# Kernel tuning notes

Measured on AMD Instinct MI355X. Metric: run time of the kernel, lower is better.

Reference implementation:

```python
import jax, jax.numpy as jnp
import numpy as np

EPS = 1e-5  # torch nn.LayerNorm default

def layer_norm(x, g, b):
    mu = jnp.mean(x, axis=-1, keepdims=True)
    var = jnp.mean((x - mu) ** 2, axis=-1, keepdims=True)  # biased, as torch
    return (x - mu) * jax.lax.rsqrt(var + EPS) * g + b

def quantum_circuit(v):
    # RX(v_w) per wire -> <Z_w> = cos(v_w); RZ(params) is diagonal phase (no effect
    # on Z probabilities); CNOT chain makes bit w = XOR of bits 0..w, hence
    # <Z_w> = prod_{k<=w} cos(v_k). Exact closed form of the PennyLane circuit.
    return jnp.cumprod(jnp.cos(v), axis=-1)

def setup_inputs() -> dict:
    key = jax.random.key(0)
    ks = jax.random.split(key, 8)
    B, T, C, H = 4, 2048, 1024, 16
    dk = C // H           # n_qubits_transformer
    nq_ffn, ffn_dim = 16, 4096
    return {
        "x": jax.random.normal(ks[0], (B, T, C), dtype=jnp.float32) * 0.5,
        "attn_circuit_params": jax.random.normal(ks[1], (H, dk), dtype=jnp.float32),
        "ffn_circuit_params": jax.random.normal(ks[2], (nq_ffn,), dtype=jnp.float32),
        "w1": jax.random.normal(ks[3], (ffn_dim, nq_ffn), dtype=jnp.float32) * 0.1,
        "b1": jnp.zeros((ffn_dim,), dtype=jnp.float32),
        "w2": jax.random.normal(ks[4], (C, ffn_dim), dtype=jnp.float32) * 0.02,
        "b2": jnp.zeros((C,), dtype=jnp.float32),
        "gamma1": jnp.ones((C,), dtype=jnp.float32),
        "beta1": jnp.zeros((C,), dtype=jnp.float32),
        "gamma2": jnp.ones((C,), dtype=jnp.float32),
        "beta2": jnp.zeros((C,), dtype=jnp.float32),
    }

def reference(x, attn_circuit_params, ffn_circuit_params, w1, b1, w2, b2,
              gamma1, beta1, gamma2, beta2):
    B, T, C = x.shape
    H, dk = attn_circuit_params.shape  # dk == n_qubits_transformer == C // H
    nq = ffn_circuit_params.shape[0]
    # --- quantum attention: per-head circuit over d_k wires (RZ params drop out) ---
    xh = x.reshape(B, T, H, dk)
    attn_out = quantum_circuit(xh).reshape(B, T, C)
    x1 = layer_norm(x + attn_out, gamma1, beta1)  # dropout = identity (eval)
    # --- quantum FFN: circuit on first nq channels of each token ---
    q = quantum_circuit(x1[..., :nq])                      # [B,T,nq]
    h = jnp.einsum('btq,fq->btf', q, w1) + b1              # [B,T,ffn_dim]
    ffn_out = jnp.einsum('btf,cf->btc', jax.nn.relu(h), w2) + b2
    return layer_norm(x1 + ffn_out, gamma2, beta2)
```

## Files before the change

### kernel.cpp

```cpp
#include <hip/hip_runtime.h>

#define M_TOK 8192
#define C_DIM 1024
#define F_DIM 4096
#define NQ    16

typedef __attribute__((ext_vector_type(8))) short short8v;
typedef __attribute__((ext_vector_type(4))) float f32x4;

typedef __attribute__((address_space(1))) void as1_void;
typedef __attribute__((address_space(3))) void as3_void;

__device__ __forceinline__ void gld_lds16(const void* g, void* l) {
  __builtin_amdgcn_global_load_lds((as1_void*)g, (as3_void*)l, 16, 0, 0);
}

__device__ __forceinline__ unsigned short f2bf(float f) {
  unsigned int u = __float_as_uint(f);
  u += 0x7FFFu + ((u >> 16) & 1u);
  return (unsigned short)(u >> 16);
}

__device__ __forceinline__ void mfma_16x16x32_bf16(f32x4& d, short8v a, short8v b) {
  asm("v_mfma_f32_16x16x32_bf16 %0, %1, %2, %0" : "+v"(d) : "v"(a), "v"(b));
}

__global__ __launch_bounds__(256) void k_attn_ln1(
    const float* __restrict__ x, const float* __restrict__ g1,
    const float* __restrict__ be1, float* __restrict__ x1,
    float* __restrict__ qf) {
  const int row  = blockIdx.x;
  const int tid  = threadIdx.x;
  const int lane = tid & 63;
  const int w    = tid >> 6;
  const float* xr = x + (size_t)row * C_DIM;

  float y[4];
  float s1 = 0.f, s2 = 0.f;
#pragma unroll
  for (int hi = 0; hi < 4; ++hi) {
    const int idx = (w * 4 + hi) * 64 + lane;
    const float v = xr[idx];
    float p = cosf(v);
#pragma unroll
    for (int off = 1; off < 64; off <<= 1) {
      const float up = __shfl_up(p, off, 64);
      if (lane >= off) p *= up;
    }
    const float yy = v + p;
    y[hi] = yy;
    s1 += yy;
    s2 += yy * yy;
  }
#pragma unroll
  for (int off = 32; off; off >>= 1) {
    s1 += __shfl_xor(s1, off, 64);
    s2 += __shfl_xor(s2, off, 64);
  }
  __shared__ float red[8];
  if (lane == 0) { red[w] = s1; red[4 + w] = s2; }
  __syncthreads();
  s1 = red[0] + red[1] + red[2] + red[3];
  s2 = red[4] + red[5] + red[6] + red[7];
  const float mu  = s1 * (1.f / C_DIM);
  const float var = s2 * (1.f / C_DIM) - mu * mu;
  const float rs  = rsqrtf(var + 1e-5f);

  float* x1r = x1 + (size_t)row * C_DIM;
#pragma unroll
  for (int hi = 0; hi < 4; ++hi) {
    const int idx = (w * 4 + hi) * 64 + lane;
    const float xv = (y[hi] - mu) * rs * g1[idx] + be1[idx];
    x1r[idx] = xv;
    if (w == 0 && hi == 0) {
      const float c = cosf(xv);
      float run = 1.f, mine = 0.f;
#pragma unroll
      for (int k = 0; k < NQ; ++k) {
        const float ck = __shfl(c, k, 64);
        run *= ck;
        if (lane == k) mine = run;
      }
      if (lane < NQ) qf[(size_t)row * NQ + lane] = mine;
    }
  }
}

__global__ __launch_bounds__(256) void k_w2cast(const float* __restrict__ w2,
                                                unsigned short* __restrict__ w2b) {
  const int n4 = C_DIM * F_DIM / 4;
  for (int i = blockIdx.x * 256 + threadIdx.x; i < n4; i += gridDim.x * 256) {
    const float4 v = ((const float4*)w2)[i];
    unsigned long long pk = (unsigned long long)f2bf(v.x)
                          | ((unsigned long long)f2bf(v.y) << 16)
                          | ((unsigned long long)f2bf(v.z) << 32)
                          | ((unsigned long long)f2bf(v.w) << 48);
    ((unsigned long long*)w2b)[i] = pk;
  }
}

__global__ __launch_bounds__(256) void k_ffn1(
    const float* __restrict__ qf, const float* __restrict__ w1,
    const float* __restrict__ b1, unsigned short* __restrict__ R) {
  const int tid  = threadIdx.x;
  const int lane = tid & 63;
  const int wv   = tid >> 6;
  const int r16  = lane & 15;
  const int hk   = lane >> 4;
  const int mb   = blockIdx.x * 16;
  const int fb   = blockIdx.y * 64 + wv * 16;

  short8v a = short8v{0,0,0,0,0,0,0,0};
  short8v b = short8v{0,0,0,0,0,0,0,0};
  if (hk < 2) {
    const float* qa = qf + (size_t)(mb + r16) * NQ + hk * 8;
    const float4 a0 = *(const float4*)(qa);
    const float4 a1 = *(const float4*)(qa + 4);
    a[0] = (short)f2bf(a0.x); a[1] = (short)f2bf(a0.y);
    a[2] = (short)f2bf(a0.z); a[3] = (short)f2bf(a0.w);
    a[4] = (short)f2bf(a1.x); a[5] = (short)f2bf(a1.y);
    a[6] = (short)f2bf(a1.z); a[7] = (short)f2bf(a1.w);
    const float* wb = w1 + (size_t)(fb + r16) * NQ + hk * 8;
    const float4 b0 = *(const float4*)(wb);
    const float4 b1v = *(const float4*)(wb + 4);
    b[0] = (short)f2bf(b0.x); b[1] = (short)f2bf(b0.y);
    b[2] = (short)f2bf(b0.z); b[3] = (short)f2bf(b0.w);
    b[4] = (short)f2bf(b1v.x); b[5] = (short)f2bf(b1v.y);
    b[6] = (short)f2bf(b1v.z); b[7] = (short)f2bf(b1v.w);
  }

  f32x4 acc = {0.f, 0.f, 0.f, 0.f};
  mfma_16x16x32_bf16(acc, a, b);

  const int f = fb + r16;
  const float bn = b1[f];
#pragma unroll
  for (int r = 0; r < 4; ++r) {
    const int m = mb + hk * 4 + r;
    R[(size_t)m * F_DIM + f] = f2bf(fmaxf(acc[r] + bn, 0.f));
  }
}

#define BM 256
#define BN 128
#define BK 64
#define NT (F_DIM / BK)
#define ATILE (BM * BK)
#define BTILE (BN * BK)
#define TILE3 (ATILE + BTILE)

__global__ __launch_bounds__(512) void k_gemm(
    const unsigned short* __restrict__ R, const unsigned short* __restrict__ W2,
    const float* __restrict__ b2, float* __restrict__ xio, int m_off) {
  __shared__ unsigned short L[3 * TILE3];
  const int tid = threadIdx.x;
  const int m0 = blockIdx.x * BM;
  const int n0 = blockIdx.y * BN;
  const unsigned short* Ag = R + (size_t)m0 * F_DIM;
  const unsigned short* Bg = W2 + (size_t)n0 * F_DIM;

  const int lane = tid & 63;
  const int wv  = tid >> 6;
  const int wr  = wv >> 1;
  const int wc  = wv & 1;
  const int r16 = lane & 15;
  const int hk  = lane >> 4;
  const int ar0 = wr * 64 + r16;
  const int br0 = wc * 64 + r16;

  f32x4 acc[4][4];
  const f32x4 fzero = {0.f, 0.f, 0.f, 0.f};
#pragma unroll
  for (int i = 0; i < 4; ++i)
#pragma unroll
    for (int j = 0; j < 4; ++j) acc[i][j] = fzero;

  auto stageA = [&](int c, int t, int l) {
    const int idx = l * 512 + tid;
    const int row = idx >> 3, slot = idx & 7;
    gld_lds16(Ag + (size_t)row * F_DIM + t * BK + ((slot ^ (row & 7)) << 3),
              &L[c * TILE3 + idx * 8]);
  };
  auto stageB = [&](int c, int t, int l) {
    const int idx = l * 512 + tid;
    const int row = idx >> 3, slot = idx & 7;
    gld_lds16(Bg + (size_t)row * F_DIM + t * BK + ((slot ^ (row & 7)) << 3),
              &L[c * TILE3 + ATILE + idx * 8]);
  };
  auto rdA = [&](int c, int row, int ks) {
    return *(const short8v*)&L[c * TILE3 + row * BK + ((ks ^ (row & 7)) << 3)];
  };
  auto rdB = [&](int c, int row, int ks) {
    return *(const short8v*)&L[c * TILE3 + ATILE + row * BK + ((ks ^ (row & 7)) << 3)];
  };

#pragma unroll
  for (int l = 0; l < 4; ++l) stageA(0, 0, l);
#pragma unroll
  for (int l = 0; l < 2; ++l) stageB(0, 0, l);
#pragma unroll
  for (int l = 0; l < 4; ++l) stageA(1, 1, l);
#pragma unroll
  for (int l = 0; l < 2; ++l) stageB(1, 1, l);
  asm volatile("s_waitcnt vmcnt(6)" ::: "memory");
  __builtin_amdgcn_s_barrier();

  for (int t = 0; t < NT; ++t) {
    const int cur = t % 3;
    const int nx2 = (t + 2) % 3;
    const bool pf = (t + 2) < NT;
    short8v a[4], b[4];

#pragma unroll
    for (int i = 0; i < 4; ++i) a[i] = rdA(cur, ar0 + i * 16, hk);
#pragma unroll
    for (int j = 0; j < 4; ++j) b[j] = rdB(cur, br0 + j * 16, hk);
    if (pf) { stageA(nx2, t + 2, 0); stageA(nx2, t + 2, 1); stageB(nx2, t + 2, 0); }
    __builtin_amdgcn_s_barrier();
    __builtin_amdgcn_s_setprio(1);
#pragma unroll
    for (int i = 0; i < 4; ++i)
#pragma unroll
      for (int j = 0; j < 4; ++j)
        mfma_16x16x32_bf16(acc[i][j], a[i], b[j]);
    __builtin_amdgcn_s_setprio(0);
    __builtin_amdgcn_s_barrier();

#pragma unroll
    for (int i = 0; i < 4; ++i) a[i] = rdA(cur, ar0 + i * 16, hk + 4);
#pragma unroll
    for (int j = 0; j < 4; ++j) b[j] = rdB(cur, br0 + j * 16, hk + 4);
    if (pf) { stageA(nx2, t + 2, 2); stageA(nx2, t + 2, 3); stageB(nx2, t + 2, 1); }
    __builtin_amdgcn_s_barrier();
    __builtin_amdgcn_s_setprio(1);
#pragma unroll
    for (int i = 0; i < 4; ++i)
#pragma unroll
      for (int j = 0; j < 4; ++j)
        mfma_16x16x32_bf16(acc[i][j], a[i], b[j]);
    __builtin_amdgcn_s_setprio(0);
    if (pf) asm volatile("s_waitcnt vmcnt(6)" ::: "memory");
    else    asm volatile("s_waitcnt vmcnt(0)" ::: "memory");
    __builtin_amdgcn_s_barrier();
  }

#pragma unroll
  for (int i = 0; i < 4; ++i) {
    const int gm = m_off + m0 + wr * 64 + i * 16 + hk * 4;
#pragma unroll
    for (int j = 0; j < 4; ++j) {
      const int n = n0 + wc * 64 + j * 16 + r16;
      const float bn = b2[n];
#pragma unroll
      for (int r = 0; r < 4; ++r) {
        const size_t off = (size_t)(gm + r) * C_DIM + n;
        xio[off] = acc[i][j][r] + bn + xio[off];
      }
    }
  }
}

__global__ __launch_bounds__(256) void k_ln2(float* __restrict__ y,
                                             const float* __restrict__ g2,
                                             const float* __restrict__ be2) {
  const int row = blockIdx.x;
  const int tid = threadIdx.x;
  float* yr = y + (size_t)row * C_DIM;
  const float4 v = ((const float4*)yr)[tid];
  float s1 = v.x + v.y + v.z + v.w;
  float s2 = v.x * v.x + v.y * v.y + v.z * v.z + v.w * v.w;
#pragma unroll
  for (int off = 32; off; off >>= 1) {
    s1 += __shfl_xor(s1, off, 64);
    s2 += __shfl_xor(s2, off, 64);
  }
  __shared__ float red[8];
  const int lane = tid & 63, w = tid >> 6;
  if (lane == 0) { red[w] = s1; red[4 + w] = s2; }
  __syncthreads();
  s1 = red[0] + red[1] + red[2] + red[3];
  s2 = red[4] + red[5] + red[6] + red[7];
  const float mu  = s1 * (1.f / C_DIM);
  const float var = s2 * (1.f / C_DIM) - mu * mu;
  const float rs  = rsqrtf(var + 1e-5f);
  const float4 g = ((const float4*)g2)[tid];
  const float4 b = ((const float4*)be2)[tid];
  float4 o;
  o.x = (v.x - mu) * rs * g.x + b.x;
  o.y = (v.y - mu) * rs * g.y + b.y;
  o.z = (v.z - mu) * rs * g.z + b.z;
  o.w = (v.w - mu) * rs * g.w + b.w;
  ((float4*)yr)[tid] = o;
}

extern "C" void kernel_launch(void* const* d_in, const int* in_sizes, int n_in,
                              void* d_out, int out_size, void* d_ws, size_t ws_size,
                              hipStream_t stream) {
  const float* x   = (const float*)d_in[0];
  const float* w1  = (const float*)d_in[3];
  const float* b1  = (const float*)d_in[4];
  const float* w2  = (const float*)d_in[5];
  const float* b2  = (const float*)d_in[6];
  const float* g1  = (const float*)d_in[7];
  const float* be1 = (const float*)d_in[8];
  const float* g2  = (const float*)d_in[9];
  const float* be2 = (const float*)d_in[10];
  float* out = (float*)d_out;

  char* ws = (char*)d_ws;
  float* qf = (float*)ws;
  unsigned short* w2b = (unsigned short*)(ws + 512 * 1024);
  const size_t rbase = 512 * 1024 + (size_t)8 * 1024 * 1024;
  unsigned short* Rb = (unsigned short*)(ws + rbase);

  int cm = M_TOK;
  const size_t avail = (ws_size > rbase) ? ws_size - rbase : 0;
  const size_t need = (size_t)M_TOK * F_DIM * 2;
  if (avail < need) {
    size_t rows = (avail / ((size_t)F_DIM * 2)) & ~(size_t)255;
    cm = (rows < 256) ? 256 : (int)rows;
  }

  k_attn_ln1<<<M_TOK, 256, 0, stream>>>(x, g1, be1, out, qf);
  k_w2cast<<<2048, 256, 0, stream>>>(w2, w2b);
  for (int c0 = 0; c0 < M_TOK; c0 += cm) {
    const int cur = (M_TOK - c0 < cm) ? (M_TOK - c0) : cm;
    k_ffn1<<<dim3(cur / 16, F_DIM / 64), 256, 0, stream>>>(
        qf + (size_t)c0 * NQ, w1, b1, Rb);
    k_gemm<<<dim3(cur / BM, C_DIM / BN), 512, 0, stream>>>(Rb, w2b, b2, out, c0);
  }
  k_ln2<<<M_TOK, 256, 0, stream>>>(out, g2, be2);
}
```

Measured before the change: 145.3 us.

## Split K across wave groups in the FFN GEMM and reduce through LDS

The waves of the second FFN GEMM are reorganised into two K-groups. Each group covers half of every BK slice and computes a 128x64 output sub-tile, instead of every wave computing a 64x64 sub-tile over the full BK. This cuts the LDS fragment reads per MFMA, issues all prefetch loads in one place, and removes a barrier from each K iteration. In exchange, the epilogue gains a cross-wave reduction through LDS and a __syncthreads. The accumulator doubles to 32 f32x4 per wave, which raises register pressure.

```diff
diff --git a/kernel.cpp b/kernel.cpp
--- a/kernel.cpp
+++ b/kernel.cpp
@@ -161,17 +161,20 @@
 
   const int lane = tid & 63;
   const int wv  = tid >> 6;
-  const int wr  = wv >> 1;
-  const int wc  = wv & 1;
+  const int kz  = wv >> 2;
+  const int wq  = wv & 3;
+  const int wr  = wq >> 1;
+  const int wc  = wq & 1;
   const int r16 = lane & 15;
   const int hk  = lane >> 4;
-  const int ar0 = wr * 64 + r16;
+  const int ks  = hk + kz * 4;
+  const int ar0 = wr * 128 + r16;
   const int br0 = wc * 64 + r16;
 
-  f32x4 acc[4][4];
+  f32x4 acc[8][4];
   const f32x4 fzero = {0.f, 0.f, 0.f, 0.f};
 #pragma unroll
-  for (int i = 0; i < 4; ++i)
+  for (int i = 0; i < 8; ++i)
 #pragma unroll
     for (int j = 0; j < 4; ++j) acc[i][j] = fzero;
 
@@ -187,11 +190,11 @@
     gld_lds16(Bg + (size_t)row * F_DIM + t * BK + ((slot ^ (row & 7)) << 3),
               &L[c * TILE3 + ATILE + idx * 8]);
   };
-  auto rdA = [&](int c, int row, int ks) {
-    return *(const short8v*)&L[c * TILE3 + row * BK + ((ks ^ (row & 7)) << 3)];
+  auto rdA = [&](int c, int row, int kg) {
+    return *(const short8v*)&L[c * TILE3 + row * BK + ((kg ^ (row & 7)) << 3)];
   };
-  auto rdB = [&](int c, int row, int ks) {
-    return *(const short8v*)&L[c * TILE3 + ATILE + row * BK + ((ks ^ (row & 7)) << 3)];
+  auto rdB = [&](int c, int row, int kg) {
+    return *(const short8v*)&L[c * TILE3 + ATILE + row * BK + ((kg ^ (row & 7)) << 3)];
   };
 
 #pragma unroll
@@ -209,32 +212,20 @@
     const int cur = t % 3;
     const int nx2 = (t + 2) % 3;
     const bool pf = (t + 2) < NT;
-    short8v a[4], b[4];
-
-#pragma unroll
-    for (int i = 0; i < 4; ++i) a[i] = rdA(cur, ar0 + i * 16, hk);
-#pragma unroll
-    for (int j = 0; j < 4; ++j) b[j] = rdB(cur, br0 + j * 16, hk);
-    if (pf) { stageA(nx2, t + 2, 0); stageA(nx2, t + 2, 1); stageB(nx2, t + 2, 0); }
-    __builtin_amdgcn_s_barrier();
+    short8v a[8], b[4];
+
+#pragma unroll
+    for (int i = 0; i < 8; ++i) a[i] = rdA(cur, ar0 + i * 16, ks);
+#pragma unroll
+    for (int j = 0; j < 4; ++j) b[j] = rdB(cur, br0 + j * 16, ks);
+    if (pf) {
+      stageA(nx2, t + 2, 0); stageA(nx2, t + 2, 1);
+      stageA(nx2, t + 2, 2); stageA(nx2, t + 2, 3);
+      stageB(nx2, t + 2, 0); stageB(nx2, t + 2, 1);
+    }
     __builtin_amdgcn_s_setprio(1);
 #pragma unroll
-    for (int i = 0; i < 4; ++i)
-#pragma unroll
-      for (int j = 0; j < 4; ++j)
-        mfma_16x16x32_bf16(acc[i][j], a[i], b[j]);
-    __builtin_amdgcn_s_setprio(0);
-    __builtin_amdgcn_s_barrier();
-
-#pragma unroll
-    for (int i = 0; i < 4; ++i) a[i] = rdA(cur, ar0 + i * 16, hk + 4);
-#pragma unroll
-    for (int j = 0; j < 4; ++j) b[j] = rdB(cur, br0 + j * 16, hk + 4);
-    if (pf) { stageA(nx2, t + 2, 2); stageA(nx2, t + 2, 3); stageB(nx2, t + 2, 1); }
-    __builtin_amdgcn_s_barrier();
-    __builtin_amdgcn_s_setprio(1);
-#pragma unroll
-    for (int i = 0; i < 4; ++i)
+    for (int i = 0; i < 8; ++i)
 #pragma unroll
       for (int j = 0; j < 4; ++j)
         mfma_16x16x32_bf16(acc[i][j], a[i], b[j]);
@@ -244,17 +235,32 @@
     __builtin_amdgcn_s_barrier();
   }
 
-#pragma unroll
-  for (int i = 0; i < 4; ++i) {
-    const int gm = m_off + m0 + wr * 64 + i * 16 + hk * 4;
-#pragma unroll
-    for (int j = 0; j < 4; ++j) {
-      const int n = n0 + wc * 64 + j * 16 + r16;
-      const float bn = b2[n];
-#pragma unroll
-      for (int r = 0; r < 4; ++r) {
-        const size_t off = (size_t)(gm + r) * C_DIM + n;
-        xio[off] = acc[i][j][r] + bn + xio[off];
+  float* Lf = (float*)L;
+  if (kz == 1) {
+#pragma unroll
+    for (int i = 0; i < 8; ++i)
+#pragma unroll
+      for (int j = 0; j < 4; ++j)
+#pragma unroll
+        for (int r = 0; r < 4; ++r)
+          Lf[wq * 8192 + (i * 16 + hk * 4 + r) * 64 + j * 16 + r16] = acc[i][j][r];
+  }
+  __syncthreads();
+
+  if (kz == 0) {
+#pragma unroll
+    for (int i = 0; i < 8; ++i) {
+      const int gm = m_off + m0 + wr * 128 + i * 16 + hk * 4;
+#pragma unroll
+      for (int j = 0; j < 4; ++j) {
+        const int n = n0 + wc * 64 + j * 16 + r16;
+        const float bn = b2[n];
+#pragma unroll
+        for (int r = 0; r < 4; ++r) {
+          const float part = Lf[wq * 8192 + (i * 16 + hk * 4 + r) * 64 + j * 16 + r16];
+          const size_t off = (size_t)(gm + r) * C_DIM + n;
+          xio[off] = acc[i][j][r] + part + bn + xio[off];
+        }
       }
     }
   }
```

New measurement: 140.0 us. -3.6%, faster.
